# Kernel optimization log

Measured on AMD Instinct MI355X. Metric: run time of the kernel, lower is better.

Reference implementation:

```python
import jax, jax.numpy as jnp
import numpy as np

B, T, NCH, NBIN, NBAND = 2, 400, 8, 512, 40
NPV = NCH * NCH


def setup_inputs() -> dict:
    key = jax.random.key(0)
    ks = jax.random.split(key, 7)
    bins_real = jax.random.normal(ks[0], (B, T, NCH, NBIN), jnp.float32)
    bins_imag = jax.random.normal(ks[1], (B, T, NCH, NBIN), jnp.float32)
    band_matrix_real = jax.random.normal(ks[2], (NBIN, NBAND), jnp.float32) * 0.05
    band_matrix_imag = jax.random.normal(ks[3], (NBIN, NBAND), jnp.float32) * 0.05
    cov_to_pv_real = jax.random.normal(ks[4], (NPV, NCH * NCH), jnp.float32) * 0.1
    cov_to_pv_imag = jax.random.normal(ks[5], (NPV, NCH * NCH), jnp.float32) * 0.1
    tau = jax.random.uniform(ks[6], (NBAND,), jnp.float32, 0.8, 0.99)
    return {
        'bins_real': bins_real, 'bins_imag': bins_imag,
        'band_matrix_real': band_matrix_real, 'band_matrix_imag': band_matrix_imag,
        'cov_to_pv_real': cov_to_pv_real, 'cov_to_pv_imag': cov_to_pv_imag,
        'tau': tau,
    }


def _power_vector(bins_real, bins_imag, band_matrix_real, band_matrix_imag,
                  cov_to_pv_real, cov_to_pv_imag, tau):
    x = jax.lax.complex(bins_real, bins_imag)            # (B,T,C,F)
    nch = x.shape[-2]
    EPS = 1e-20
    # per-bin covariance outer product, flattened cov dim: (B,T,F,C*C)
    cov = jnp.einsum('btif,btjf->btfij', x, jnp.conj(x))
    b, t, f = cov.shape[:3]
    cov = cov.reshape(b, t, f, nch * nch)
    diag = jnp.arange(nch) * (nch + 1)                   # diagonal indices in cov dim
    trace = jnp.clip(jnp.sum(cov.real[..., diag], axis=-1, keepdims=True), EPS, None)
    cov = cov / trace                                    # per-bin trace normalisation
    # phase adjustment along the bin axis (n=1 -> lag of 2 bins)
    c = jnp.swapaxes(cov, -1, -2)                        # (B,T,C2,F)
    prod = jnp.conj(c[..., :-2]) * c[..., 2:]
    ang = jnp.arctan2(prod.imag, prod.real)
    ang = jnp.concatenate([ang[..., :1], ang, ang[..., -1:]], axis=-1)  # edge pad
    adj = jnp.abs(c) * jax.lax.complex(jnp.cos(ang), jnp.sin(ang))
    adj = adj.at[..., diag, :].set(c[..., diag, :])      # keep original diagonals
    # band projection: contract bins against (F,K) band matrix
    bm = jax.lax.complex(band_matrix_real, band_matrix_imag)
    band_cov = jnp.einsum('btcf,fk->btkc', adj, bm)      # (B,T,K,C2)
    dsum = jnp.clip(band_cov.real[..., diag].sum(-1, keepdims=True), EPS, None)
    band_cov = band_cov / dsum
    # first-order IIR smoothing over frames, per-band pole tau
    a = tau[:, None].astype(band_cov.real.dtype)         # (K,1)
    def step(carry, xt):
        y = a * carry + (1.0 - a) * xt
        return y, y
    y0 = jnp.zeros_like(band_cov[:, 0])                  # (B,K,C2)
    _, ys = jax.lax.scan(step, y0, jnp.moveaxis(band_cov, 1, 0))
    band_cov = jnp.moveaxis(ys, 0, 1)                    # (B,T,K,C2)
    # cov -> power vector projection, real part
    c2p = jax.lax.complex(cov_to_pv_real, cov_to_pv_imag)  # (P,C2)
    pv = jnp.einsum('pc,btkc->btkp', c2p, band_cov).real   # (B,T,K,P)
    return pv


def reference(bins_real, bins_imag, band_matrix_real, band_matrix_imag,
              cov_to_pv_real, cov_to_pv_imag, tau):
    return _power_vector(bins_real, bins_imag, band_matrix_real, band_matrix_imag,
                         cov_to_pv_real, cov_to_pv_imag, tau)
```

## Files before the change

### kernel.cpp

```cpp
#include <hip/hip_runtime.h>
#include <hip/hip_fp16.h>

#define B_    2
#define T_    400
#define NCH_  8
#define NBIN_ 512
#define NBAND_ 40
#define NPV_  64

using half8   = __attribute__((ext_vector_type(8))) _Float16;
using float4v = __attribute__((ext_vector_type(4))) float;

static __device__ inline unsigned pkhf(float x, float y) {
  __half2 h = __float22half2_rn(make_float2(x, y));
  return __builtin_bit_cast(unsigned, h);
}
static __device__ inline unsigned rot16(unsigned u) {
  return (u >> 16) | (u << 16);
}
static __device__ inline unsigned cmulc(unsigned viu, unsigned vju) {
  __half2 Vi = __builtin_bit_cast(__half2, viu);
  __half2 Vj = __builtin_bit_cast(__half2, vju);
  __half2 P1 = __hmul2(Vi, __low2half2(Vj));
  __half2 Qi = __lowhigh2highlow(Vi);
  unsigned tn = __builtin_bit_cast(unsigned, __high2half2(Vj)) ^ 0x80000000u;
  __half2 a  = __hfma2(Qi, __builtin_bit_cast(__half2, tn), P1);
  return __builtin_bit_cast(unsigned, a);
}

__global__ __launch_bounds__(256) void pv_prep(
    const float* __restrict__ bmr, const float* __restrict__ bmi,
    const float* __restrict__ c2pr, const float* __restrict__ c2pi,
    float* __restrict__ ws)
{
  const int tid = threadIdx.x;
  const int blk = blockIdx.x;
  if (blk == 0) {
    __shared__ float sds[256];
    int k = tid & 63, part = tid >> 6;
    float s = 0.f;
    if (k < NBAND_) {
      const float* col = bmr + k;
      #pragma unroll 16
      for (int f = part * 128; f < part * 128 + 128; f++) s += col[f * 40];
    }
    sds[tid] = s;
    __syncthreads();
    if (tid < NBAND_) {
      float t = sds[tid] + sds[tid + 64] + sds[tid + 128] + sds[tid + 192];
      ws[tid] = 1.0f / fmaxf(t, 1e-20f);
    }
  } else if (blk <= 24) {
    int F = (blk - 1) * 256 + tid;
    int l = F & 63;
    int fid = F >> 6;
    int s5 = fid / 3;
    int n = fid - s5 * 3;
    int k = n * 16 + (l & 15);
    int quad = l >> 4;
    unsigned dw[4];
    #pragma unroll
    for (int t2 = 0; t2 < 4; t2++) {
      float v0 = 0.f, v1 = 0.f;
      if (k < NBAND_) {
        int f = s5 * 16 + quad * 4 + t2;
        v0 = bmr[f * 40 + k]; v1 = bmi[f * 40 + k];
      }
      dw[t2] = pkhf(v0, v1);
    }
    ((uint4*)((char*)ws + 1024))[F] = make_uint4(dw[0], dw[1], dw[2], dw[3]);
  } else {
    int F2 = (blk - 25) * 256 + tid;
    int lane = F2 & 63, E = F2 >> 6;
    int nt = E >> 2, ks = E & 3;
    int n = lane & 15, quad = lane >> 4;
    int p = nt * 16 + n;
    unsigned dw[4];
    #pragma unroll
    for (int t2 = 0; t2 < 4; t2++) {
      int c = ks * 16 + quad * 4 + t2;
      dw[t2] = pkhf(c2pr[p * 64 + c], -c2pi[p * 64 + c]);
    }
    ((uint4*)((char*)ws + 197632))[E * 64 + lane] = make_uint4(dw[0], dw[1], dw[2], dw[3]);
  }
}

__global__ __launch_bounds__(256, 4) void pv_main(
    const float* __restrict__ br, const float* __restrict__ bi,
    const float* __restrict__ ws, float* __restrict__ out)
{
  __shared__ __align__(16) unsigned smem[4096];

  const int bt  = blockIdx.x;
  const int tid = threadIdx.x;

  const int mt   = tid >> 6;
  const int lane = tid & 63;
  const int m16  = lane & 15;
  const int quad = lane >> 4;
  const int p    = mt * 16 + m16;
  const int ich  = p >> 3, jch = p & 7;
  const uint4* BF0 = (const uint4*)((const char*)ws + 1024);

  {
    const float* pr  = br + (size_t)bt * (NCH_ * NBIN_);
    const float* pim = bi + (size_t)bt * (NCH_ * NBIN_);
    unsigned* vsh = smem;
    #pragma unroll
    for (int fs = 0; fs < 2; fs++) {
      const int f = fs * 256 + tid;
      const int fm = (f == 0) ? 0 : ((f == 511) ? 509 : f - 1);
      const int fp = (f == 0) ? 2 : ((f == 511) ? 511 : f + 1);
      float tr = 0.f;
      float t1[8], t2[8];
      #pragma unroll
      for (int c = 0; c < 8; c++) {
        const float* cr = pr + c * 512;
        const float* ci = pim + c * 512;
        float xr = cr[f],   xi = ci[f];
        float xrm = cr[fm], xim = ci[fm];
        float xrp = cr[fp], xip = ci[fp];
        tr = fmaf(xr, xr, tr); tr = fmaf(xi, xi, tr);
        float Gr = fmaf(xrm, xrp,  xim * xip);
        float Gi = fmaf(xrm, xip, -(xim * xrp));
        float am = fmaxf(fmaxf(fabsf(Gr), fabsf(Gi)), 1e-30f);
        float rc = __builtin_amdgcn_rcpf(am);
        float q1 = Gr * rc, q2 = Gi * rc;
        float n2 = fmaf(q1, q1, q2 * q2);
        float rn = __builtin_amdgcn_rsqf(n2);
        bool ok = n2 > 0.f;
        float ur = ok ? q1 * rn : 1.f;
        float ui = ok ? q2 * rn : 0.f;
        float mg = __builtin_amdgcn_sqrtf(fmaf(xr, xr, xi * xi));
        t1[c] = mg * ur; t2[c] = mg * ui;
      }
      float scv = __builtin_amdgcn_rsqf(fmaxf(tr, 1e-20f));
      const int fc = f >> 2, fl = f & 3;
      #pragma unroll
      for (int c = 0; c < 8; c++)
        vsh[c * 512 + ((fc ^ c) << 2) + fl] = pkhf(t1[c] * scv, t2[c] * scv);
    }
  }
  __syncthreads();

  float4v acc[6];
  #pragma unroll
  for (int g = 0; g < 6; g++) acc[g] = (float4v){0.f, 0.f, 0.f, 0.f};

  const uint4* Bg = BF0 + lane;
  uint4 nb0 = Bg[0], nb1 = Bg[64], nb2 = Bg[128];
  #pragma unroll 4
  for (int s = 0; s < 32; s++) {
    uint4 cb0 = nb0, cb1 = nb1, cb2 = nb2;
    {
      const uint4* nx = Bg + (size_t)(((s + 1) & 31) * 192);
      nb0 = nx[0]; nb1 = nx[64]; nb2 = nx[128];
    }
    const int sc = s * 4 + quad;
    half8 b0 = __builtin_bit_cast(half8, cb0);
    half8 b1 = __builtin_bit_cast(half8, cb1);
    half8 b2 = __builtin_bit_cast(half8, cb2);
    const uint4* vb = (const uint4*)smem;
    uint4 av = vb[ich * 128 + (sc ^ ich)];
    uint4 bv = vb[jch * 128 + (sc ^ jch)];
    unsigned a0 = cmulc(av.x, bv.x);
    unsigned a1 = cmulc(av.y, bv.y);
    unsigned a2 = cmulc(av.z, bv.z);
    unsigned a3 = cmulc(av.w, bv.w);
    uint4 au1 = make_uint4(a0 ^ 0x80000000u, a1 ^ 0x80000000u,
                           a2 ^ 0x80000000u, a3 ^ 0x80000000u);
    uint4 au2 = make_uint4(rot16(a0), rot16(a1),
                           rot16(a2), rot16(a3));
    half8 af1 = __builtin_bit_cast(half8, au1);
    half8 af2 = __builtin_bit_cast(half8, au2);
    acc[0] = __builtin_amdgcn_mfma_f32_16x16x32_f16(af1, b0, acc[0], 0, 0, 0);
    acc[3] = __builtin_amdgcn_mfma_f32_16x16x32_f16(af2, b0, acc[3], 0, 0, 0);
    acc[1] = __builtin_amdgcn_mfma_f32_16x16x32_f16(af1, b1, acc[1], 0, 0, 0);
    acc[4] = __builtin_amdgcn_mfma_f32_16x16x32_f16(af2, b1, acc[4], 0, 0, 0);
    acc[2] = __builtin_amdgcn_mfma_f32_16x16x32_f16(af1, b2, acc[2], 0, 0, 0);
    acc[5] = __builtin_amdgcn_mfma_f32_16x16x32_f16(af2, b2, acc[5], 0, 0, 0);
  }
  __syncthreads();

  const uint4* EF = ((const uint4*)((const char*)ws + 197632)) + (mt * 4) * 64 + lane;
  uint4 eb[4];
  #pragma unroll
  for (int ks = 0; ks < 4; ks++) eb[ks] = EF[ks * 64];

  {
    unsigned* bcsh = smem;
    #pragma unroll
    for (int n = 0; n < 3; n++) {
      uint4 w4 = make_uint4(pkhf(acc[n][0], acc[n+3][0]),
                            pkhf(acc[n][1], acc[n+3][1]),
                            pkhf(acc[n][2], acc[n+3][2]),
                            pkhf(acc[n][3], acc[n+3][3]));
      *(uint4*)(bcsh + (n * 16 + m16) * 68 + mt * 16 + quad * 4) = w4;
    }
  }
  __syncthreads();

  const float4* wsd = (const float4*)ws;
  {
    const unsigned* bcsh = smem;
    float4v eacc[3];
    #pragma unroll
    for (int kt = 0; kt < 3; kt++) eacc[kt] = (float4v){0.f, 0.f, 0.f, 0.f};
    #pragma unroll
    for (int ks = 0; ks < 4; ks++) {
      half8 bfr = __builtin_bit_cast(half8, eb[ks]);
      #pragma unroll
      for (int kt = 0; kt < 3; kt++) {
        uint4 a4 = *(const uint4*)(bcsh + (kt * 16 + m16) * 68 + ks * 16 + quad * 4);
        half8 afr = __builtin_bit_cast(half8, a4);
        eacc[kt] = __builtin_amdgcn_mfma_f32_16x16x32_f16(afr, bfr, eacc[kt], 0, 0, 0);
      }
    }
    float* op = out + (size_t)bt * (NBAND_ * NPV_);
    #pragma unroll
    for (int kt = 0; kt < 3; kt++) {
      float4 dv = wsd[kt * 4 + quad];
      float dva[4] = {dv.x, dv.y, dv.z, dv.w};
      #pragma unroll
      for (int r = 0; r < 4; r++) {
        int k = kt * 16 + quad * 4 + r;
        if (k < NBAND_)
          op[k * 64 + mt * 16 + m16] = eacc[kt][r] * dva[r];
      }
    }
  }
}

__global__ __launch_bounds__(640) void pv_iir4(float* __restrict__ z,
                                               const float* __restrict__ tau)
{
  __shared__ float gsh[40][16];
  const int pg = blockIdx.x & 3;
  const int bk = blockIdx.x >> 2;
  const int k = bk % NBAND_;
  const int b = bk / NBAND_;
  const float a  = tau[k];
  const float om = 1.0f - a;
  const int c  = threadIdx.x >> 4;
  const int pl = threadIdx.x & 15;
  const int p  = pg * 16 + pl;
  const size_t stride = (size_t)NBAND_ * 64;
  size_t idx0 = (size_t)b * (T_ * NBAND_ * 64) + (size_t)(c * 10) * stride + k * 64 + p;

  float y[10];
  float accv = 0.f;
  #pragma unroll
  for (int i = 0; i < 10; i++) {
    float v = z[idx0 + (size_t)i * stride];
    accv = fmaf(a, accv, om * v);
    y[i] = accv;
  }
  gsh[c][pl] = accv;
  __syncthreads();
  float a2 = a * a, a4 = a2 * a2, a8 = a4 * a4;
  float A = a8 * a2;
  float H = 0.f;
  #pragma unroll
  for (int d = 0; d < 39; d++) {
    float g = gsh[d][pl];
    H = (d < c) ? fmaf(A, H, g) : H;
  }
  float wp = a;
  #pragma unroll
  for (int i = 0; i < 10; i++) {
    z[idx0 + (size_t)i * stride] = fmaf(wp, H, y[i]);
    wp *= a;
  }
}

extern "C" void kernel_launch(void* const* d_in, const int* in_sizes, int n_in,
                              void* d_out, int out_size, void* d_ws, size_t ws_size,
                              hipStream_t stream)
{
  const float* br   = (const float*)d_in[0];
  const float* bi   = (const float*)d_in[1];
  const float* bmr  = (const float*)d_in[2];
  const float* bmi  = (const float*)d_in[3];
  const float* c2pr = (const float*)d_in[4];
  const float* c2pi = (const float*)d_in[5];
  const float* tau  = (const float*)d_in[6];
  float* out = (float*)d_out;
  float* ws  = (float*)d_ws;

  hipLaunchKernelGGL(pv_prep, dim3(29), dim3(256), 0, stream,
                     bmr, bmi, c2pr, c2pi, ws);
  hipLaunchKernelGGL(pv_main, dim3(B_ * T_), dim3(256), 0, stream,
                     br, bi, ws, out);
  hipLaunchKernelGGL(pv_iir4, dim3(B_ * NBAND_ * 4), dim3(640), 0, stream,
                     out, tau);
}
```

Baseline: 118.8 us.

## Process two bins per thread with vector loads and deepen B-fragment prefetch

The prologue now has each thread handle two adjacent bins, reading a float4 window per channel so neighbour values are shared instead of re-loaded with scalar gathers, and writes packed uint2 to shared memory. Edge threads keep the original scalar path. The main MFMA loop prefetches B fragments two iterations ahead instead of one to hide global load latency, and launch bounds drop from 4 to 3 waves-per-SIMD to make room for the extra registers. The cost is higher register pressure and lower occupancy.

```diff
diff --git a/kernel.cpp b/kernel.cpp
--- a/kernel.cpp
+++ b/kernel.cpp
@@ -85,7 +85,7 @@
   }
 }
 
-__global__ __launch_bounds__(256, 4) void pv_main(
+__global__ __launch_bounds__(256, 3) void pv_main(
     const float* __restrict__ br, const float* __restrict__ bi,
     const float* __restrict__ ws, float* __restrict__ out)
 {
@@ -106,39 +106,97 @@
     const float* pr  = br + (size_t)bt * (NCH_ * NBIN_);
     const float* pim = bi + (size_t)bt * (NCH_ * NBIN_);
     unsigned* vsh = smem;
-    #pragma unroll
-    for (int fs = 0; fs < 2; fs++) {
-      const int f = fs * 256 + tid;
-      const int fm = (f == 0) ? 0 : ((f == 511) ? 509 : f - 1);
-      const int fp = (f == 0) ? 2 : ((f == 511) ? 511 : f + 1);
-      float tr = 0.f;
-      float t1[8], t2[8];
+    const int f0 = 2 * tid;
+    if (tid == 0 || tid == 255) {
+      #pragma unroll
+      for (int bb = 0; bb < 2; bb++) {
+        const int f = f0 + bb;
+        const int fm = (f == 0) ? 0 : ((f == 511) ? 509 : f - 1);
+        const int fp = (f == 0) ? 2 : ((f == 511) ? 511 : f + 1);
+        float tr = 0.f;
+        float t1[8], t2[8];
+        #pragma unroll
+        for (int c = 0; c < 8; c++) {
+          const float* cr = pr + c * 512;
+          const float* ci = pim + c * 512;
+          float xr = cr[f],   xi = ci[f];
+          float xrm = cr[fm], xim = ci[fm];
+          float xrp = cr[fp], xip = ci[fp];
+          tr = fmaf(xr, xr, tr); tr = fmaf(xi, xi, tr);
+          float Gr = fmaf(xrm, xrp,  xim * xip);
+          float Gi = fmaf(xrm, xip, -(xim * xrp));
+          float am = fmaxf(fmaxf(fabsf(Gr), fabsf(Gi)), 1e-30f);
+          float rc = __builtin_amdgcn_rcpf(am);
+          float q1 = Gr * rc, q2 = Gi * rc;
+          float n2 = fmaf(q1, q1, q2 * q2);
+          float rn = __builtin_amdgcn_rsqf(n2);
+          bool ok = n2 > 0.f;
+          float ur = ok ? q1 * rn : 1.f;
+          float ui = ok ? q2 * rn : 0.f;
+          float mg = __builtin_amdgcn_sqrtf(fmaf(xr, xr, xi * xi));
+          t1[c] = mg * ur; t2[c] = mg * ui;
+        }
+        float scv = __builtin_amdgcn_rsqf(fmaxf(tr, 1e-20f));
+        const int fc = f >> 2, fl = f & 3;
+        #pragma unroll
+        for (int c = 0; c < 8; c++)
+          vsh[c * 512 + ((fc ^ c) << 2) + fl] = pkhf(t1[c] * scv, t2[c] * scv);
+      }
+    } else {
+      const int base = f0 - 1;
+      float tra = 0.f, trb = 0.f;
+      float t1a[8], t2a[8], t1b[8], t2b[8];
       #pragma unroll
       for (int c = 0; c < 8; c++) {
-        const float* cr = pr + c * 512;
-        const float* ci = pim + c * 512;
-        float xr = cr[f],   xi = ci[f];
-        float xrm = cr[fm], xim = ci[fm];
-        float xrp = cr[fp], xip = ci[fp];
-        tr = fmaf(xr, xr, tr); tr = fmaf(xi, xi, tr);
-        float Gr = fmaf(xrm, xrp,  xim * xip);
-        float Gi = fmaf(xrm, xip, -(xim * xrp));
-        float am = fmaxf(fmaxf(fabsf(Gr), fabsf(Gi)), 1e-30f);
-        float rc = __builtin_amdgcn_rcpf(am);
-        float q1 = Gr * rc, q2 = Gi * rc;
-        float n2 = fmaf(q1, q1, q2 * q2);
-        float rn = __builtin_amdgcn_rsqf(n2);
-        bool ok = n2 > 0.f;
-        float ur = ok ? q1 * rn : 1.f;
-        float ui = ok ? q2 * rn : 0.f;
-        float mg = __builtin_amdgcn_sqrtf(fmaf(xr, xr, xi * xi));
-        t1[c] = mg * ur; t2[c] = mg * ui;
-      }
-      float scv = __builtin_amdgcn_rsqf(fmaxf(tr, 1e-20f));
-      const int fc = f >> 2, fl = f & 3;
-      #pragma unroll
-      for (int c = 0; c < 8; c++)
-        vsh[c * 512 + ((fc ^ c) << 2) + fl] = pkhf(t1[c] * scv, t2[c] * scv);
+        float4 wr, wi;
+        __builtin_memcpy(&wr, pr + c * 512 + base, 16);
+        __builtin_memcpy(&wi, pim + c * 512 + base, 16);
+        {
+          float xr = wr.y, xi = wi.y;
+          float xrm = wr.x, xim = wi.x;
+          float xrp = wr.z, xip = wi.z;
+          tra = fmaf(xr, xr, tra); tra = fmaf(xi, xi, tra);
+          float Gr = fmaf(xrm, xrp,  xim * xip);
+          float Gi = fmaf(xrm, xip, -(xim * xrp));
+          float am = fmaxf(fmaxf(fabsf(Gr), fabsf(Gi)), 1e-30f);
+          float rc = __builtin_amdgcn_rcpf(am);
+          float q1 = Gr * rc, q2 = Gi * rc;
+          float n2 = fmaf(q1, q1, q2 * q2);
+          float rn = __builtin_amdgcn_rsqf(n2);
+          bool ok = n2 > 0.f;
+          float ur = ok ? q1 * rn : 1.f;
+          float ui = ok ? q2 * rn : 0.f;
+          float mg = __builtin_amdgcn_sqrtf(fmaf(xr, xr, xi * xi));
+          t1a[c] = mg * ur; t2a[c] = mg * ui;
+        }
+        {
+          float xr = wr.z, xi = wi.z;
+          float xrm = wr.y, xim = wi.y;
+          float xrp = wr.w, xip = wi.w;
+          trb = fmaf(xr, xr, trb); trb = fmaf(xi, xi, trb);
+          float Gr = fmaf(xrm, xrp,  xim * xip);
+          float Gi = fmaf(xrm, xip, -(xim * xrp));
+          float am = fmaxf(fmaxf(fabsf(Gr), fabsf(Gi)), 1e-30f);
+          float rc = __builtin_amdgcn_rcpf(am);
+          float q1 = Gr * rc, q2 = Gi * rc;
+          float n2 = fmaf(q1, q1, q2 * q2);
+          float rn = __builtin_amdgcn_rsqf(n2);
+          bool ok = n2 > 0.f;
+          float ur = ok ? q1 * rn : 1.f;
+          float ui = ok ? q2 * rn : 0.f;
+          float mg = __builtin_amdgcn_sqrtf(fmaf(xr, xr, xi * xi));
+          t1b[c] = mg * ur; t2b[c] = mg * ui;
+        }
+      }
+      float scva = __builtin_amdgcn_rsqf(fmaxf(tra, 1e-20f));
+      float scvb = __builtin_amdgcn_rsqf(fmaxf(trb, 1e-20f));
+      const int fc = f0 >> 2, fl = f0 & 3;
+      #pragma unroll
+      for (int c = 0; c < 8; c++) {
+        unsigned d0 = pkhf(t1a[c] * scva, t2a[c] * scva);
+        unsigned d1 = pkhf(t1b[c] * scvb, t2b[c] * scvb);
+        *(uint2*)(vsh + c * 512 + ((fc ^ c) << 2) + fl) = make_uint2(d0, d1);
+      }
     }
   }
   __syncthreads();
@@ -148,13 +206,15 @@
   for (int g = 0; g < 6; g++) acc[g] = (float4v){0.f, 0.f, 0.f, 0.f};
 
   const uint4* Bg = BF0 + lane;
-  uint4 nb0 = Bg[0], nb1 = Bg[64], nb2 = Bg[128];
+  uint4 pa0 = Bg[0],   pa1 = Bg[64],  pa2 = Bg[128];
+  uint4 pb0 = Bg[192], pb1 = Bg[256], pb2 = Bg[320];
   #pragma unroll 4
   for (int s = 0; s < 32; s++) {
-    uint4 cb0 = nb0, cb1 = nb1, cb2 = nb2;
+    uint4 cb0 = pa0, cb1 = pa1, cb2 = pa2;
+    pa0 = pb0; pa1 = pb1; pa2 = pb2;
     {
-      const uint4* nx = Bg + (size_t)(((s + 1) & 31) * 192);
-      nb0 = nx[0]; nb1 = nx[64]; nb2 = nx[128];
+      const uint4* nx = Bg + (size_t)(((s + 2) & 31) * 192);
+      pb0 = nx[0]; pb1 = nx[64]; pb2 = nx[128];
     }
     const int sc = s * 4 + quad;
     half8 b0 = __builtin_bit_cast(half8, cb0);
```

After: 112.3 us. 1.06x faster.

## Split band-projection K loop across two wave groups with 512-thread blocks

Applied to the files above, without the earlier changes.

The main kernel now launches 512 threads per block. Each thread computes one bin's phase-adjusted vector, loading its neighbours with 16-byte vector loads instead of six scalar gathers. Two groups of four waves each take half of the 32 K-steps of the MFMA band projection, and their partial accumulators are summed through extra shared memory before the cov-to-pv projection. This halves the serial MFMA chain per wave and raises parallelism, at the cost of more LDS (40KB), an extra reduction pass with a barrier, and idle waves during the epilogue.

```diff
diff --git a/kernel.cpp b/kernel.cpp
--- a/kernel.cpp
+++ b/kernel.cpp
@@ -85,16 +85,18 @@
   }
 }
 
-__global__ __launch_bounds__(256, 4) void pv_main(
+__global__ __launch_bounds__(512, 4) void pv_main(
     const float* __restrict__ br, const float* __restrict__ bi,
     const float* __restrict__ ws, float* __restrict__ out)
 {
-  __shared__ __align__(16) unsigned smem[4096];
+  __shared__ __align__(16) unsigned smem[10240];
 
   const int bt  = blockIdx.x;
   const int tid = threadIdx.x;
 
-  const int mt   = tid >> 6;
+  const int w     = tid >> 6;
+  const int mt    = w & 3;
+  const int sBase = (w >> 2) * 16;
   const int lane = tid & 63;
   const int m16  = lane & 15;
   const int quad = lane >> 4;
@@ -106,9 +108,8 @@
     const float* pr  = br + (size_t)bt * (NCH_ * NBIN_);
     const float* pim = bi + (size_t)bt * (NCH_ * NBIN_);
     unsigned* vsh = smem;
-    #pragma unroll
-    for (int fs = 0; fs < 2; fs++) {
-      const int f = fs * 256 + tid;
+    const int f = tid;
+    if (f == 0 || f >= 510) {
       const int fm = (f == 0) ? 0 : ((f == 511) ? 509 : f - 1);
       const int fp = (f == 0) ? 2 : ((f == 511) ? 511 : f + 1);
       float tr = 0.f;
@@ -139,6 +140,39 @@
       #pragma unroll
       for (int c = 0; c < 8; c++)
         vsh[c * 512 + ((fc ^ c) << 2) + fl] = pkhf(t1[c] * scv, t2[c] * scv);
+    } else {
+      float4 wr[8], wi[8];
+      #pragma unroll
+      for (int c = 0; c < 8; c++) {
+        __builtin_memcpy(&wr[c], pr + c * 512 + (f - 1), 16);
+        __builtin_memcpy(&wi[c], pim + c * 512 + (f - 1), 16);
+      }
+      float tr = 0.f;
+      float t1[8], t2[8];
+      #pragma unroll
+      for (int c = 0; c < 8; c++) {
+        float xr = wr[c].y, xi = wi[c].y;
+        float xrm = wr[c].x, xim = wi[c].x;
+        float xrp = wr[c].z, xip = wi[c].z;
+        tr = fmaf(xr, xr, tr); tr = fmaf(xi, xi, tr);
+        float Gr = fmaf(xrm, xrp,  xim * xip);
+        float Gi = fmaf(xrm, xip, -(xim * xrp));
+        float am = fmaxf(fmaxf(fabsf(Gr), fabsf(Gi)), 1e-30f);
+        float rc = __builtin_amdgcn_rcpf(am);
+        float q1 = Gr * rc, q2 = Gi * rc;
+        float n2 = fmaf(q1, q1, q2 * q2);
+        float rn = __builtin_amdgcn_rsqf(n2);
+        bool ok = n2 > 0.f;
+        float ur = ok ? q1 * rn : 1.f;
+        float ui = ok ? q2 * rn : 0.f;
+        float mg = __builtin_amdgcn_sqrtf(fmaf(xr, xr, xi * xi));
+        t1[c] = mg * ur; t2[c] = mg * ui;
+      }
+      float scv = __builtin_amdgcn_rsqf(fmaxf(tr, 1e-20f));
+      const int fc = f >> 2, fl = f & 3;
+      #pragma unroll
+      for (int c = 0; c < 8; c++)
+        vsh[c * 512 + ((fc ^ c) << 2) + fl] = pkhf(t1[c] * scv, t2[c] * scv);
     }
   }
   __syncthreads();
@@ -148,13 +182,21 @@
   for (int g = 0; g < 6; g++) acc[g] = (float4v){0.f, 0.f, 0.f, 0.f};
 
   const uint4* Bg = BF0 + lane;
-  uint4 nb0 = Bg[0], nb1 = Bg[64], nb2 = Bg[128];
+  uint4 pa0 = Bg[(size_t)(sBase + 0) * 192],
+        pa1 = Bg[(size_t)(sBase + 0) * 192 + 64],
+        pa2 = Bg[(size_t)(sBase + 0) * 192 + 128];
+  uint4 pb0 = Bg[(size_t)(sBase + 1) * 192],
+        pb1 = Bg[(size_t)(sBase + 1) * 192 + 64],
+        pb2 = Bg[(size_t)(sBase + 1) * 192 + 128];
   #pragma unroll 4
-  for (int s = 0; s < 32; s++) {
-    uint4 cb0 = nb0, cb1 = nb1, cb2 = nb2;
+  for (int t = 0; t < 16; t++) {
+    const int s = sBase + t;
+    uint4 cb0 = pa0, cb1 = pa1, cb2 = pa2;
+    pa0 = pb0; pa1 = pb1; pa2 = pb2;
     {
-      const uint4* nx = Bg + (size_t)(((s + 1) & 31) * 192);
-      nb0 = nx[0]; nb1 = nx[64]; nb2 = nx[128];
+      const int s2 = sBase + ((t + 2) & 15);
+      const uint4* nx = Bg + (size_t)s2 * 192;
+      pb0 = nx[0]; pb1 = nx[64]; pb2 = nx[128];
     }
     const int sc = s * 4 + quad;
     half8 b0 = __builtin_bit_cast(half8, cb0);
@@ -180,14 +222,21 @@
     acc[2] = __builtin_amdgcn_mfma_f32_16x16x32_f16(af1, b2, acc[2], 0, 0, 0);
     acc[5] = __builtin_amdgcn_mfma_f32_16x16x32_f16(af2, b2, acc[5], 0, 0, 0);
   }
+
+  uint4* red = (uint4*)(smem + 4096);
+  if (w >= 4) {
+    #pragma unroll
+    for (int g = 0; g < 6; g++)
+      red[((size_t)(w - 4) * 64 + lane) * 6 + g] = __builtin_bit_cast(uint4, acc[g]);
+  }
   __syncthreads();
 
-  const uint4* EF = ((const uint4*)((const char*)ws + 197632)) + (mt * 4) * 64 + lane;
-  uint4 eb[4];
-  #pragma unroll
-  for (int ks = 0; ks < 4; ks++) eb[ks] = EF[ks * 64];
-
-  {
+  if (w < 4) {
+    #pragma unroll
+    for (int g = 0; g < 6; g++) {
+      float4v o = __builtin_bit_cast(float4v, red[((size_t)w * 64 + lane) * 6 + g]);
+      acc[g] += o;
+    }
     unsigned* bcsh = smem;
     #pragma unroll
     for (int n = 0; n < 3; n++) {
@@ -200,9 +249,14 @@
   }
   __syncthreads();
 
-  const float4* wsd = (const float4*)ws;
-  {
+  if (w < 4) {
+    const uint4* EF = ((const uint4*)((const char*)ws + 197632)) + (mt * 4) * 64 + lane;
+    uint4 eb[4];
+    #pragma unroll
+    for (int ks = 0; ks < 4; ks++) eb[ks] = EF[ks * 64];
+
     const unsigned* bcsh = smem;
+    const float4* wsd = (const float4*)ws;
     float4v eacc[3];
     #pragma unroll
     for (int kt = 0; kt < 3; kt++) eacc[kt] = (float4v){0.f, 0.f, 0.f, 0.f};
@@ -289,7 +343,7 @@
 
   hipLaunchKernelGGL(pv_prep, dim3(29), dim3(256), 0, stream,
                      bmr, bmi, c2pr, c2pi, ws);
-  hipLaunchKernelGGL(pv_main, dim3(B_ * T_), dim3(256), 0, stream,
+  hipLaunchKernelGGL(pv_main, dim3(B_ * T_), dim3(512), 0, stream,
                      br, bi, ws, out);
   hipLaunchKernelGGL(pv_iir4, dim3(B_ * NBAND_ * 4), dim3(640), 0, stream,
                      out, tau);
```

Measured after the change: 115.6 us. 2.7% less time.

## Stage input bins in LDS, deepen B-fragment prefetch, reshape IIR scan blocks

Applied to the files above, without the earlier changes.

The main kernel now copies each frame's real and imaginary bins into shared memory with coalesced float4 loads, then reads the neighbour bins (f-1, f, f+1) from LDS instead of making three scattered global reads per channel. The B-fragment prefetch is deepened from one stage to two to hide global latency in the MFMA loop. The IIR kernel is reshaped to 16 chunks of 25 frames with 32 columns per block, which shortens the cross-chunk carry loop. In exchange, LDS use triples to 48KB per block, launch bounds drop to 3 blocks per CU, and more registers are live.

```diff
diff --git a/kernel.cpp b/kernel.cpp
--- a/kernel.cpp
+++ b/kernel.cpp
@@ -85,11 +85,11 @@
   }
 }
 
-__global__ __launch_bounds__(256, 4) void pv_main(
+__global__ __launch_bounds__(256, 3) void pv_main(
     const float* __restrict__ br, const float* __restrict__ bi,
     const float* __restrict__ ws, float* __restrict__ out)
 {
-  __shared__ __align__(16) unsigned smem[4096];
+  __shared__ __align__(16) unsigned smem[12288];
 
   const int bt  = blockIdx.x;
   const int tid = threadIdx.x;
@@ -101,11 +101,24 @@
   const int p    = mt * 16 + m16;
   const int ich  = p >> 3, jch = p & 7;
   const uint4* BF0 = (const uint4*)((const char*)ws + 1024);
+  unsigned* vsh = smem + 8192;
 
   {
-    const float* pr  = br + (size_t)bt * (NCH_ * NBIN_);
-    const float* pim = bi + (size_t)bt * (NCH_ * NBIN_);
-    unsigned* vsh = smem;
+    const float4* gr4 = (const float4*)(br + (size_t)bt * (NCH_ * NBIN_));
+    const float4* gi4 = (const float4*)(bi + (size_t)bt * (NCH_ * NBIN_));
+    float4* lr4 = (float4*)smem;
+    float4* li4 = (float4*)(smem + 4096);
+    #pragma unroll
+    for (int it = 0; it < 4; it++) {
+      lr4[it * 256 + tid] = gr4[it * 256 + tid];
+      li4[it * 256 + tid] = gi4[it * 256 + tid];
+    }
+  }
+  __syncthreads();
+
+  {
+    const float* rr = (const float*)smem;
+    const float* ri = (const float*)(smem + 4096);
     #pragma unroll
     for (int fs = 0; fs < 2; fs++) {
       const int f = fs * 256 + tid;
@@ -115,8 +128,8 @@
       float t1[8], t2[8];
       #pragma unroll
       for (int c = 0; c < 8; c++) {
-        const float* cr = pr + c * 512;
-        const float* ci = pim + c * 512;
+        const float* cr = rr + c * 512;
+        const float* ci = ri + c * 512;
         float xr = cr[f],   xi = ci[f];
         float xrm = cr[fm], xim = ci[fm];
         float xrp = cr[fp], xip = ci[fp];
@@ -148,19 +161,21 @@
   for (int g = 0; g < 6; g++) acc[g] = (float4v){0.f, 0.f, 0.f, 0.f};
 
   const uint4* Bg = BF0 + lane;
-  uint4 nb0 = Bg[0], nb1 = Bg[64], nb2 = Bg[128];
+  uint4 pa0 = Bg[0],   pa1 = Bg[64],  pa2 = Bg[128];
+  uint4 pb0 = Bg[192], pb1 = Bg[256], pb2 = Bg[320];
   #pragma unroll 4
   for (int s = 0; s < 32; s++) {
-    uint4 cb0 = nb0, cb1 = nb1, cb2 = nb2;
+    uint4 cb0 = pa0, cb1 = pa1, cb2 = pa2;
+    pa0 = pb0; pa1 = pb1; pa2 = pb2;
     {
-      const uint4* nx = Bg + (size_t)(((s + 1) & 31) * 192);
-      nb0 = nx[0]; nb1 = nx[64]; nb2 = nx[128];
+      const uint4* nx = Bg + (size_t)(((s + 2) & 31) * 192);
+      pb0 = nx[0]; pb1 = nx[64]; pb2 = nx[128];
     }
     const int sc = s * 4 + quad;
     half8 b0 = __builtin_bit_cast(half8, cb0);
     half8 b1 = __builtin_bit_cast(half8, cb1);
     half8 b2 = __builtin_bit_cast(half8, cb2);
-    const uint4* vb = (const uint4*)smem;
+    const uint4* vb = (const uint4*)vsh;
     uint4 av = vb[ich * 128 + (sc ^ ich)];
     uint4 bv = vb[jch * 128 + (sc ^ jch)];
     unsigned a0 = cmulc(av.x, bv.x);
@@ -231,43 +246,43 @@
   }
 }
 
-__global__ __launch_bounds__(640) void pv_iir4(float* __restrict__ z,
+__global__ __launch_bounds__(512) void pv_iir4(float* __restrict__ z,
                                                const float* __restrict__ tau)
 {
-  __shared__ float gsh[40][16];
-  const int pg = blockIdx.x & 3;
-  const int bk = blockIdx.x >> 2;
+  __shared__ float gsh[16][32];
+  const int ph = blockIdx.x & 1;
+  const int bk = blockIdx.x >> 1;
   const int k = bk % NBAND_;
   const int b = bk / NBAND_;
   const float a  = tau[k];
   const float om = 1.0f - a;
-  const int c  = threadIdx.x >> 4;
-  const int pl = threadIdx.x & 15;
-  const int p  = pg * 16 + pl;
+  const int c  = threadIdx.x >> 5;
+  const int pl = threadIdx.x & 31;
+  const int p  = ph * 32 + pl;
   const size_t stride = (size_t)NBAND_ * 64;
-  size_t idx0 = (size_t)b * (T_ * NBAND_ * 64) + (size_t)(c * 10) * stride + k * 64 + p;
-
-  float y[10];
+  size_t idx0 = (size_t)b * (T_ * NBAND_ * 64) + (size_t)(c * 25) * stride + k * 64 + p;
+
+  float y[25];
   float accv = 0.f;
   #pragma unroll
-  for (int i = 0; i < 10; i++) {
+  for (int i = 0; i < 25; i++) {
     float v = z[idx0 + (size_t)i * stride];
     accv = fmaf(a, accv, om * v);
     y[i] = accv;
   }
   gsh[c][pl] = accv;
   __syncthreads();
-  float a2 = a * a, a4 = a2 * a2, a8 = a4 * a4;
-  float A = a8 * a2;
+  float a2 = a * a, a4 = a2 * a2, a8 = a4 * a4, a16 = a8 * a8;
+  float A = a16 * a8 * a;
   float H = 0.f;
   #pragma unroll
-  for (int d = 0; d < 39; d++) {
+  for (int d = 0; d < 15; d++) {
     float g = gsh[d][pl];
     H = (d < c) ? fmaf(A, H, g) : H;
   }
   float wp = a;
   #pragma unroll
-  for (int i = 0; i < 10; i++) {
+  for (int i = 0; i < 25; i++) {
     z[idx0 + (size_t)i * stride] = fmaf(wp, H, y[i]);
     wp *= a;
   }
@@ -291,6 +306,6 @@
                      bmr, bmi, c2pr, c2pi, ws);
   hipLaunchKernelGGL(pv_main, dim3(B_ * T_), dim3(256), 0, stream,
                      br, bi, ws, out);
-  hipLaunchKernelGGL(pv_iir4, dim3(B_ * NBAND_ * 4), dim3(640), 0, stream,
+  hipLaunchKernelGGL(pv_iir4, dim3(B_ * NBAND_ * 2), dim3(512), 0, stream,
                      out, tau);
 }
```

After: 108.8 us, median of 2. 8.3% less time.
